# Optimization experiments

Hardware: AMD Instinct MI355X
Metric: run time of the kernel (lower is better)

The kernel has to match this reference:

```python
import jax, jax.numpy as jnp
import numpy as np

LOG_STD_MAX = 2.0
LOG_STD_MIN = -5.0
HEIGHT = 4          # tree height -> 16 leaves, 15 internal nodes
TOP_K = 4           # top-k leaves kept in soft gate
SMAX_TEMP = 1.0     # softmax temperature over selected leaf logits


def _path_matrix(height: int) -> np.ndarray:
    """[N_internal, L] matrix with +1 where a leaf's root-to-leaf path goes
    left through a node, -1 where it goes right, 0 otherwise."""
    L = 2 ** height
    P = np.zeros((L - 1, L), dtype=np.float32)
    for leaf in range(L):
        node = 0
        for lvl in range(height):
            bit = (leaf >> (height - 1 - lvl)) & 1
            P[node, leaf] = 1.0 if bit == 0 else -1.0
            node = 2 * node + 1 + bit
    return P


def setup_inputs() -> dict:
    key = jax.random.key(0)
    k0, k1, k2, k3, k4 = jax.random.split(key, 5)
    B, D, A = 262144, 128, 8
    L = 2 ** HEIGHT
    N = L - 1
    x = jax.random.normal(k0, (B, D), dtype=jnp.float32)
    Wn = jax.random.normal(k1, (D, N), dtype=jnp.float32) / np.float32(np.sqrt(D))
    bn = jax.random.normal(k2, (N,), dtype=jnp.float32) * 0.01
    Wl = jax.random.normal(k3, (L, D, 2 * A), dtype=jnp.float32) / np.float32(np.sqrt(D))
    bl = jax.random.normal(k4, (L, 2 * A), dtype=jnp.float32) * 0.01
    return {"x": x, "Wn": Wn, "bn": bn, "Wl": Wl, "bl": bl}


def reference(x, Wn, bn, Wl, bl):
    L = Wl.shape[0]
    P = jnp.asarray(_path_matrix(HEIGHT))              # [N, L] constant

    # --- differentiable-tree routing ---
    node_logits = x @ Wn + bn                          # [B, N]
    leaf_logits = node_logits @ P                      # [B, L]
    vals, idx = jax.lax.top_k(leaf_logits, TOP_K)      # [B, k]
    soft = jax.nn.softmax(vals / SMAX_TEMP, axis=-1)   # [B, k]
    onehot = jax.nn.one_hot(idx, L, dtype=x.dtype)     # [B, k, L]
    gate_soft = jnp.einsum('bk,bkl->bl', soft, onehot) # scatter soft weights
    gate_hard = onehot[:, 0]                           # argmax leaf one-hot
    # hard argmax forward, top-k softmax gradient (straight-through)
    gate = gate_hard + gate_soft - jax.lax.stop_gradient(gate_soft)

    # --- per-leaf linear controllers, gated sum ---
    leaf_out = jnp.einsum('bd,ldo->blo', x, Wl) + bl   # [B, L, 2A]
    out = jnp.einsum('bl,blo->bo', gate, leaf_out)     # [B, 2A]

    A = out.shape[-1] // 2
    mean, log_std = out[:, :A], out[:, A:]
    log_std = jnp.tanh(log_std)
    log_std = LOG_STD_MIN + 0.5 * (LOG_STD_MAX - LOG_STD_MIN) * (log_std + 1.0)
    return mean, log_std
```

## Files before the change

### kernel.cpp

```cpp
#include <hip/hip_runtime.h>
#include <math.h>

#define BLK  256
#define DD   128
#define NN   15
#define NL   16
#define OC   16
#define OSTR 20
#define GAPTHR 1e-3f

typedef __attribute__((ext_vector_type(8))) short short8v;
typedef __attribute__((ext_vector_type(4))) float f32x4;
typedef union { unsigned u[4]; short8v s; } fragu;

__device__ inline unsigned bf16_rne_u(float f) {
    unsigned u = __float_as_uint(f);
    return (u + 0x7FFFu + ((u >> 16) & 1u)) >> 16;
}
__device__ inline unsigned cvt_pk_bf16(float a, float b) {
    unsigned r;
    asm volatile("v_cvt_pk_bf16_f32 %0, %1, %2" : "=v"(r) : "v"(a), "v"(b));
    return r;
}
__device__ inline void split8(const float v[8], short8v& hi, short8v& lo) {
    fragu H, L;
    #pragma unroll
    for (int p = 0; p < 4; ++p) {
        const float a = v[2*p], b = v[2*p+1];
        const unsigned h = cvt_pk_bf16(a, b);
        H.u[p] = h;
        const float ra = a - __uint_as_float(h << 16);
        const float rb = b - __uint_as_float(h & 0xFFFF0000u);
        L.u[p] = cvt_pk_bf16(ra, rb);
    }
    hi = H.s; lo = L.s;
}

__global__ __launch_bounds__(256)
void dts_prep(const float* __restrict__ Wn, const float* __restrict__ Wl,
              unsigned short* __restrict__ wlB,
              unsigned short* __restrict__ wnHi, unsigned short* __restrict__ wnLo)
{
    const int id = blockIdx.x * 256 + threadIdx.x;
    if (id < 32768) {
        const int j = id & 7, n = (id >> 3) & 15, g = (id >> 7) & 3,
                  c = (id >> 9) & 3, leaf = id >> 11;
        const int k = c * 32 + g * 8 + j;
        wlB[id] = (unsigned short)bf16_rne_u(Wl[((size_t)leaf * DD + k) * OC + n]);
    } else if (id < 32768 + 2048) {
        const int id2 = id - 32768;
        const int j = id2 & 7, n = (id2 >> 3) & 15, g = (id2 >> 7) & 3, c = id2 >> 9;
        const int k = c * 32 + g * 8 + j;
        const float v = (n < NN) ? Wn[k * NN + n] : 0.f;
        const unsigned hb = bf16_rne_u(v);
        wnHi[id2] = (unsigned short)hb;
        wnLo[id2] = (unsigned short)bf16_rne_u(v - __uint_as_float(hb << 16));
    }
}

__global__ __launch_bounds__(BLK, 3)
void dts_fused11(const float* __restrict__ x, const float* __restrict__ Wn,
                 const float* __restrict__ bn, const float* __restrict__ bl,
                 const unsigned short* __restrict__ wlB,
                 const unsigned short* __restrict__ wnHi,
                 const unsigned short* __restrict__ wnLo,
                 float* __restrict__ out, int B)
{
    __shared__ __align__(16) float sXch[BLK * OSTR];
    __shared__ float sBn[NN];
    __shared__ __align__(16) float sBl[NL * OC];
    __shared__ unsigned char sLeaf[BLK];

    const int t    = threadIdx.x;
    const int wv   = t >> 6;
    const int lane = t & 63;
    const int lo16 = t & 15;
    const int grp  = (t >> 4) & 3;
    const int rowBase = blockIdx.x * BLK;

    if (t < NN) sBn[t] = bn[t];
    for (int i = t; i < NL * OC; i += BLK) sBl[i] = bl[i];
    __syncthreads();

    const int waveRow0 = rowBase + wv * 64;
    short8v ah[4][4];
    f32x4 accn[4];
    #pragma unroll
    for (int i = 0; i < 4; ++i) accn[i] = (f32x4){0.f, 0.f, 0.f, 0.f};

    #pragma unroll
    for (int c = 0; c < 4; ++c) {
        const short8v bh = *(const short8v*)&wnHi[(c * 64 + lane) * 8];
        const short8v bw = *(const short8v*)&wnLo[(c * 64 + lane) * 8];
        #pragma unroll
        for (int i = 0; i < 4; ++i) {
            const float* ap = x + (size_t)(waveRow0 + i * 16 + lo16) * DD + c * 32 + grp * 8;
            const float4 a0 = *(const float4*)ap;
            const float4 a1 = *(const float4*)(ap + 4);
            float av[8];
            av[0]=a0.x; av[1]=a0.y; av[2]=a0.z; av[3]=a0.w;
            av[4]=a1.x; av[5]=a1.y; av[6]=a1.z; av[7]=a1.w;
            short8v hi, lo;
            split8(av, hi, lo);
            ah[c][i] = hi;
            accn[i] = __builtin_amdgcn_mfma_f32_16x16x32_bf16(hi, bh, accn[i], 0, 0, 0);
            accn[i] = __builtin_amdgcn_mfma_f32_16x16x32_bf16(lo, bh, accn[i], 0, 0, 0);
            accn[i] = __builtin_amdgcn_mfma_f32_16x16x32_bf16(hi, bw, accn[i], 0, 0, 0);
        }
        __builtin_amdgcn_sched_barrier(0);
    }

    {
        float* patch = &sXch[wv * 64 * OSTR];
        #pragma unroll
        for (int i = 0; i < 4; ++i)
            #pragma unroll
            for (int j = 0; j < 4; ++j)
                patch[(i * 16 + grp * 4 + j) * OSTR + lo16] = accn[i][j];
    }
    asm volatile("s_waitcnt lgkmcnt(0)" ::: "memory");
    __builtin_amdgcn_sched_barrier(0);

    float nl[16];
    {
        const float4* np = (const float4*)&sXch[t * OSTR];
        const float4 n0 = np[0], n1 = np[1], n2 = np[2], n3 = np[3];
        nl[0]=n0.x; nl[1]=n0.y; nl[2]=n0.z;  nl[3]=n0.w;
        nl[4]=n1.x; nl[5]=n1.y; nl[6]=n1.z;  nl[7]=n1.w;
        nl[8]=n2.x; nl[9]=n2.y; nl[10]=n2.z; nl[11]=n2.w;
        nl[12]=n3.x; nl[13]=n3.y; nl[14]=n3.z;
    }
    #pragma unroll
    for (int n = 0; n < NN; ++n) nl[n] += sBn[n];

    float L2a[4], L3a[8], L4a[16];
    #define EXPAND(src) { \
        float p = src[0], m = -src[0]; \
        L2a[0] = p + src[1]; L2a[1] = p - src[1]; \
        L2a[2] = m + src[2]; L2a[3] = m - src[2]; \
        _Pragma("unroll") \
        for (int i = 0; i < 4; ++i) { L3a[2*i] = L2a[i] + src[3+i]; L3a[2*i+1] = L2a[i] - src[3+i]; } \
        _Pragma("unroll") \
        for (int i = 0; i < 8; ++i) { L4a[2*i] = L3a[i] + src[7+i]; L4a[2*i+1] = L3a[i] - src[7+i]; } }
    EXPAND(nl)
    int best = 0; float bv = L4a[0], sv = -1e30f;
    #pragma unroll
    for (int l = 1; l < NL; ++l) {
        if (L4a[l] > bv) { sv = bv; bv = L4a[l]; best = l; }
        else if (L4a[l] > sv) sv = L4a[l];
    }

    if (bv - sv < GAPTHR) {
        float e[NN];
        #pragma unroll
        for (int n = 0; n < NN; ++n) e[n] = 0.f;
        const float* xrow = x + (size_t)(rowBase + t) * DD;
        for (int d = 0; d < DD; ++d) {
            const float xd = xrow[d];
            const float* wr = Wn + d * NN;
            #pragma unroll
            for (int n = 0; n < NN; ++n) e[n] = fmaf(xd, wr[n], e[n]);
        }
        #pragma unroll
        for (int n = 0; n < NN; ++n) e[n] += sBn[n];
        EXPAND(e)
        best = 0; bv = L4a[0];
        #pragma unroll
        for (int l = 1; l < NL; ++l) if (L4a[l] > bv) { bv = L4a[l]; best = l; }
    }
    #undef EXPAND

    sLeaf[t] = (unsigned char)best;
    asm volatile("s_waitcnt lgkmcnt(0)" ::: "memory");
    __builtin_amdgcn_sched_barrier(0);

    unsigned lfp[4];
    #pragma unroll
    for (int rt = 0; rt < 4; ++rt)
        lfp[rt] = *(const unsigned*)&sLeaf[wv * 64 + rt * 16 + grp * 4];

    f32x4 keep[4];
    #pragma unroll
    for (int rt = 0; rt < 4; ++rt) keep[rt] = (f32x4){0.f, 0.f, 0.f, 0.f};

    #pragma unroll 1
    for (int nt = 0; nt < NL; ++nt) {
        short8v bf[4];
        #pragma unroll
        for (int c = 0; c < 4; ++c)
            bf[c] = *(const short8v*)&wlB[nt * 2048 + (c * 64 + lane) * 8];
        f32x4 acc[4];
        #pragma unroll
        for (int rt = 0; rt < 4; ++rt) acc[rt] = (f32x4){0.f, 0.f, 0.f, 0.f};
        #pragma unroll
        for (int c = 0; c < 4; ++c)
            #pragma unroll
            for (int rt = 0; rt < 4; ++rt)
                acc[rt] = __builtin_amdgcn_mfma_f32_16x16x32_bf16(ah[c][rt], bf[c], acc[rt], 0, 0, 0);
        #pragma unroll
        for (int rt = 0; rt < 4; ++rt)
            #pragma unroll
            for (int j = 0; j < 4; ++j)
                keep[rt][j] = (((lfp[rt] >> (8 * j)) & 0xFFu) == (unsigned)nt)
                            ? acc[rt][j] : keep[rt][j];
    }

    {
        float* patch = &sXch[wv * 64 * OSTR];
        #pragma unroll
        for (int rt = 0; rt < 4; ++rt)
            #pragma unroll
            for (int j = 0; j < 4; ++j) {
                const int lf = (lfp[rt] >> (8 * j)) & 0xFF;
                patch[(rt * 16 + grp * 4 + j) * OSTR + lo16] =
                    keep[rt][j] + sBl[lf * OC + lo16];
            }
    }
    asm volatile("s_waitcnt lgkmcnt(0)" ::: "memory");
    __builtin_amdgcn_sched_barrier(0);
    {
        const float* so = &sXch[t * OSTR];
        const float4 m0 = *(const float4*)(so);
        const float4 m1 = *(const float4*)(so + 4);
        const float4 s0 = *(const float4*)(so + 8);
        const float4 s1 = *(const float4*)(so + 12);

        const size_t ob = (size_t)(rowBase + t) * 8;
        *reinterpret_cast<float4*>(&out[ob])     = m0;
        *reinterpret_cast<float4*>(&out[ob + 4]) = m1;

        float4 r0, r1;
        #define SQ(v) (-1.5f + 3.5f * (1.f - 2.f / (__expf(2.f * (v)) + 1.f)))
        r0.x = SQ(s0.x); r0.y = SQ(s0.y); r0.z = SQ(s0.z); r0.w = SQ(s0.w);
        r1.x = SQ(s1.x); r1.y = SQ(s1.y); r1.z = SQ(s1.z); r1.w = SQ(s1.w);
        #undef SQ
        const size_t ob2 = (size_t)B * 8 + ob;
        *reinterpret_cast<float4*>(&out[ob2])     = r0;
        *reinterpret_cast<float4*>(&out[ob2 + 4]) = r1;
    }
}

extern "C" void kernel_launch(void* const* d_in, const int* in_sizes, int n_in,
                              void* d_out, int out_size, void* d_ws, size_t ws_size,
                              hipStream_t stream)
{
    const float* x  = (const float*)d_in[0];
    const float* Wn = (const float*)d_in[1];
    const float* bn = (const float*)d_in[2];
    const float* Wl = (const float*)d_in[3];
    const float* bl = (const float*)d_in[4];
    float* out = (float*)d_out;

    unsigned short* wlB  = (unsigned short*)d_ws;
    unsigned short* wnHi = wlB + 32768;
    unsigned short* wnLo = wnHi + 2048;

    const int B = in_sizes[0] / DD;
    const int blocks = (B + BLK - 1) / BLK;

    hipLaunchKernelGGL(dts_prep, dim3(136), dim3(256), 0, stream, Wn, Wl, wlB, wnHi, wnLo);
    hipLaunchKernelGGL(dts_fused11, dim3(blocks), dim3(BLK), 0, stream,
                       x, Wn, bn, bl, wlB, wnHi, wnLo, out, B);
}
```

Baseline: 62.11 us.

## Use single-wave blocks and double-buffer leaf weight fragments across leaf loop

Shrinks the block from four waves to one, so the block barrier is replaced by a wave-local LDS wait and each wave schedules independently. The leaf loop now processes two leaves per iteration and prefetches the next leaf's bf16 weight fragments into a second register set while the current leaf's MFMAs run, hiding global-load latency. The extra fragment registers raise register pressure against the higher launch-bounds occupancy target, and four times as many blocks are launched, each staging the biases separately.

```diff
diff --git a/kernel.cpp b/kernel.cpp
--- a/kernel.cpp
+++ b/kernel.cpp
@@ -1,7 +1,7 @@
 #include <hip/hip_runtime.h>
 #include <math.h>
 
-#define BLK  256
+#define BLK  64
 #define DD   128
 #define NN   15
 #define NL   16
@@ -58,8 +58,8 @@
     }
 }
 
-__global__ __launch_bounds__(BLK, 3)
-void dts_fused11(const float* __restrict__ x, const float* __restrict__ Wn,
+__global__ __launch_bounds__(BLK, 4)
+void dts_fused12(const float* __restrict__ x, const float* __restrict__ Wn,
                  const float* __restrict__ bn, const float* __restrict__ bl,
                  const unsigned short* __restrict__ wlB,
                  const unsigned short* __restrict__ wnHi,
@@ -72,17 +72,15 @@
     __shared__ unsigned char sLeaf[BLK];
 
     const int t    = threadIdx.x;
-    const int wv   = t >> 6;
-    const int lane = t & 63;
     const int lo16 = t & 15;
-    const int grp  = (t >> 4) & 3;
+    const int grp  = t >> 4;
     const int rowBase = blockIdx.x * BLK;
 
     if (t < NN) sBn[t] = bn[t];
     for (int i = t; i < NL * OC; i += BLK) sBl[i] = bl[i];
-    __syncthreads();
-
-    const int waveRow0 = rowBase + wv * 64;
+    asm volatile("s_waitcnt lgkmcnt(0)" ::: "memory");
+    __builtin_amdgcn_sched_barrier(0);
+
     short8v ah[4][4];
     f32x4 accn[4];
     #pragma unroll
@@ -90,11 +88,11 @@
 
     #pragma unroll
     for (int c = 0; c < 4; ++c) {
-        const short8v bh = *(const short8v*)&wnHi[(c * 64 + lane) * 8];
-        const short8v bw = *(const short8v*)&wnLo[(c * 64 + lane) * 8];
+        const short8v bh = *(const short8v*)&wnHi[(c * 64 + t) * 8];
+        const short8v bw = *(const short8v*)&wnLo[(c * 64 + t) * 8];
         #pragma unroll
         for (int i = 0; i < 4; ++i) {
-            const float* ap = x + (size_t)(waveRow0 + i * 16 + lo16) * DD + c * 32 + grp * 8;
+            const float* ap = x + (size_t)(rowBase + i * 16 + lo16) * DD + c * 32 + grp * 8;
             const float4 a0 = *(const float4*)ap;
             const float4 a1 = *(const float4*)(ap + 4);
             float av[8];
@@ -110,14 +108,11 @@
         __builtin_amdgcn_sched_barrier(0);
     }
 
-    {
-        float* patch = &sXch[wv * 64 * OSTR];
-        #pragma unroll
-        for (int i = 0; i < 4; ++i)
-            #pragma unroll
-            for (int j = 0; j < 4; ++j)
-                patch[(i * 16 + grp * 4 + j) * OSTR + lo16] = accn[i][j];
-    }
+    #pragma unroll
+    for (int i = 0; i < 4; ++i)
+        #pragma unroll
+        for (int j = 0; j < 4; ++j)
+            sXch[(i * 16 + grp * 4 + j) * OSTR + lo16] = accn[i][j];
     asm volatile("s_waitcnt lgkmcnt(0)" ::: "memory");
     __builtin_amdgcn_sched_barrier(0);
 
@@ -177,45 +172,61 @@
     unsigned lfp[4];
     #pragma unroll
     for (int rt = 0; rt < 4; ++rt)
-        lfp[rt] = *(const unsigned*)&sLeaf[wv * 64 + rt * 16 + grp * 4];
+        lfp[rt] = *(const unsigned*)&sLeaf[rt * 16 + grp * 4];
 
     f32x4 keep[4];
     #pragma unroll
     for (int rt = 0; rt < 4; ++rt) keep[rt] = (f32x4){0.f, 0.f, 0.f, 0.f};
 
+    short8v bfA0, bfA1, bfA2, bfA3, bfB0, bfB1, bfB2, bfB3;
+    const int fo = t * 8;
+    bfA0 = *(const short8v*)&wlB[fo];
+    bfA1 = *(const short8v*)&wlB[ 512 + fo];
+    bfA2 = *(const short8v*)&wlB[1024 + fo];
+    bfA3 = *(const short8v*)&wlB[1536 + fo];
+
+    #define DOLEAF(nt, F0, F1, F2, F3) { \
+        f32x4 acc[4]; \
+        _Pragma("unroll") \
+        for (int rt = 0; rt < 4; ++rt) acc[rt] = (f32x4){0.f, 0.f, 0.f, 0.f}; \
+        _Pragma("unroll") \
+        for (int rt = 0; rt < 4; ++rt) { \
+            acc[rt] = __builtin_amdgcn_mfma_f32_16x16x32_bf16(ah[0][rt], F0, acc[rt], 0, 0, 0); \
+            acc[rt] = __builtin_amdgcn_mfma_f32_16x16x32_bf16(ah[1][rt], F1, acc[rt], 0, 0, 0); \
+            acc[rt] = __builtin_amdgcn_mfma_f32_16x16x32_bf16(ah[2][rt], F2, acc[rt], 0, 0, 0); \
+            acc[rt] = __builtin_amdgcn_mfma_f32_16x16x32_bf16(ah[3][rt], F3, acc[rt], 0, 0, 0); \
+        } \
+        _Pragma("unroll") \
+        for (int rt = 0; rt < 4; ++rt) \
+            _Pragma("unroll") \
+            for (int j = 0; j < 4; ++j) \
+                keep[rt][j] = (((lfp[rt] >> (8 * j)) & 0xFFu) == (unsigned)(nt)) \
+                            ? acc[rt][j] : keep[rt][j]; }
+
     #pragma unroll 1
-    for (int nt = 0; nt < NL; ++nt) {
-        short8v bf[4];
-        #pragma unroll
-        for (int c = 0; c < 4; ++c)
-            bf[c] = *(const short8v*)&wlB[nt * 2048 + (c * 64 + lane) * 8];
-        f32x4 acc[4];
-        #pragma unroll
-        for (int rt = 0; rt < 4; ++rt) acc[rt] = (f32x4){0.f, 0.f, 0.f, 0.f};
-        #pragma unroll
-        for (int c = 0; c < 4; ++c)
-            #pragma unroll
-            for (int rt = 0; rt < 4; ++rt)
-                acc[rt] = __builtin_amdgcn_mfma_f32_16x16x32_bf16(ah[c][rt], bf[c], acc[rt], 0, 0, 0);
-        #pragma unroll
-        for (int rt = 0; rt < 4; ++rt)
-            #pragma unroll
-            for (int j = 0; j < 4; ++j)
-                keep[rt][j] = (((lfp[rt] >> (8 * j)) & 0xFFu) == (unsigned)nt)
-                            ? acc[rt][j] : keep[rt][j];
-    }
-
-    {
-        float* patch = &sXch[wv * 64 * OSTR];
-        #pragma unroll
-        for (int rt = 0; rt < 4; ++rt)
-            #pragma unroll
-            for (int j = 0; j < 4; ++j) {
-                const int lf = (lfp[rt] >> (8 * j)) & 0xFF;
-                patch[(rt * 16 + grp * 4 + j) * OSTR + lo16] =
-                    keep[rt][j] + sBl[lf * OC + lo16];
-            }
-    }
+    for (int nt = 0; nt < NL; nt += 2) {
+        const int nB = nt + 1;
+        bfB0 = *(const short8v*)&wlB[nB * 2048 +        fo];
+        bfB1 = *(const short8v*)&wlB[nB * 2048 +  512 + fo];
+        bfB2 = *(const short8v*)&wlB[nB * 2048 + 1024 + fo];
+        bfB3 = *(const short8v*)&wlB[nB * 2048 + 1536 + fo];
+        DOLEAF(nt, bfA0, bfA1, bfA2, bfA3)
+        const int nA = (nt + 2 < NL) ? nt + 2 : 0;
+        bfA0 = *(const short8v*)&wlB[nA * 2048 +        fo];
+        bfA1 = *(const short8v*)&wlB[nA * 2048 +  512 + fo];
+        bfA2 = *(const short8v*)&wlB[nA * 2048 + 1024 + fo];
+        bfA3 = *(const short8v*)&wlB[nA * 2048 + 1536 + fo];
+        DOLEAF(nB, bfB0, bfB1, bfB2, bfB3)
+    }
+    #undef DOLEAF
+
+    #pragma unroll
+    for (int rt = 0; rt < 4; ++rt)
+        #pragma unroll
+        for (int j = 0; j < 4; ++j) {
+            const int lf = (lfp[rt] >> (8 * j)) & 0xFF;
+            sXch[(rt * 16 + grp * 4 + j) * OSTR + lo16] = keep[rt][j] + sBl[lf * OC + lo16];
+        }
     asm volatile("s_waitcnt lgkmcnt(0)" ::: "memory");
     __builtin_amdgcn_sched_barrier(0);
     {
@@ -259,6 +270,6 @@
     const int blocks = (B + BLK - 1) / BLK;
 
     hipLaunchKernelGGL(dts_prep, dim3(136), dim3(256), 0, stream, Wn, Wl, wlB, wnHi, wnLo);
-    hipLaunchKernelGGL(dts_fused11, dim3(blocks), dim3(BLK), 0, stream,
+    hipLaunchKernelGGL(dts_fused12, dim3(blocks), dim3(BLK), 0, stream,
                        x, Wn, bn, bl, wlB, wnHi, wnLo, out, B);
 }
```

Result: slower. 114.5 us (+84.3%).
